# Kernel tuning notes

Measured on AMD Instinct MI355X. Metric: run time of the kernel, lower is better.

## Reference

```python
import jax, jax.numpy as jnp
import numpy as np

I, H, O = 32, 64, 8  # input_size, hidden_layer, output_size
B, T = 4096, 256


def setup_inputs() -> dict:
    key = jax.random.key(0)
    ks = jax.random.split(key, 7)
    s_ih = 1.0 / np.sqrt(H)
    return {
        "x": jax.random.normal(ks[0], (B, T, I), dtype=jnp.float32),
        # PyTorch nn.LSTM params, gate order [i, f, g, o]
        "W_ih": jax.random.uniform(ks[1], (4 * H, I), jnp.float32, -s_ih, s_ih),
        "W_hh": jax.random.uniform(ks[2], (4 * H, H), jnp.float32, -s_ih, s_ih),
        "b_ih": jax.random.uniform(ks[3], (4 * H,), jnp.float32, -s_ih, s_ih),
        "b_hh": jax.random.uniform(ks[4], (4 * H,), jnp.float32, -s_ih, s_ih),
        "W_fc": jax.random.uniform(ks[5], (O, H), jnp.float32, -s_ih, s_ih),
        "b_fc": jax.random.uniform(ks[6], (O,), jnp.float32, -s_ih, s_ih),
    }


def reference(x, W_ih, W_hh, b_ih, b_hh, W_fc, b_fc):
    # Precompute input-to-hidden projections for all timesteps in one GEMM.
    # [B, T, 4H]
    x_proj = jnp.einsum('bti,gi->btg', x, W_ih) + b_ih + b_hh

    def step(carry, xp_t):
        h, c = carry  # [B, H] each
        gates = xp_t + h @ W_hh.T  # [B, 4H]
        i_g, f_g, g_g, o_g = jnp.split(gates, 4, axis=-1)
        i_g = jax.nn.sigmoid(i_g)
        f_g = jax.nn.sigmoid(f_g)
        g_g = jnp.tanh(g_g)
        o_g = jax.nn.sigmoid(o_g)
        c = f_g * c + i_g * g_g
        h = o_g * jnp.tanh(c)
        return (h, c), None

    h0 = jnp.zeros((x.shape[0], H), dtype=x.dtype)
    c0 = jnp.zeros((x.shape[0], H), dtype=x.dtype)
    # scan over time axis: move T to leading axis
    (h_T, c_T), _ = jax.lax.scan(step, (h0, c0), jnp.swapaxes(x_proj, 0, 1))
    # out[:, -1, :] == final hidden state for single-layer batch_first LSTM
    return h_T @ W_fc.T + b_fc
```

## Files before the change

### kernel.cpp

```cpp
#include <hip/hip_runtime.h>
#include <hip/hip_bf16.h>


#define T_LEN 256
#define I_SZ  32
#define H_SZ  64
#define O_SZ  8
#define BR    8
#define HS    72

typedef __attribute__((ext_vector_type(8))) short short8;
typedef __attribute__((ext_vector_type(4))) float f32x4;
typedef __attribute__((ext_vector_type(2))) float f32x2;

static __device__ __forceinline__ unsigned fbits(float f) {
    union { float f; unsigned u; } v; v.f = f; return v.u;
}
static __device__ __forceinline__ unsigned pk2t(float lo, float hi) {
    return __builtin_amdgcn_perm(fbits(hi), fbits(lo), 0x07060302u);
}
static __device__ __forceinline__ short f2bf_rne(float f) {
    union { __hip_bfloat16 b; short s; } u;
    u.b = __float2bfloat16(f);
    return u.s;
}
static __device__ __forceinline__ f32x2 rcp2(f32x2 d) {
    f32x2 r;
    r.x = __builtin_amdgcn_rcpf(d.x);
    r.y = __builtin_amdgcn_rcpf(d.y);
    return r;
}
static __device__ __forceinline__ f32x2 fma2(f32x2 a, f32x2 b, f32x2 c) {
    return __builtin_elementwise_fma(a, b, c);
}
static __device__ __forceinline__ f32x2 tanh2(f32x2 x) {
    f32x2 x2 = x * x;
    f32x2 n  = fma2(x2 + 105.0f, x2, (f32x2)(945.0f));
    f32x2 d  = fma2(fma2((f32x2)(15.0f), x2, (f32x2)(420.0f)), x2, (f32x2)(945.0f));
    f32x2 r  = (x * n) * rcp2(d);
    r = __builtin_elementwise_min(r, (f32x2)(1.0f));
    r = __builtin_elementwise_max(r, (f32x2)(-1.0f));
    return r;
}
static __device__ __forceinline__ f32x2 sig2(f32x2 x) {
    f32x2 x2 = x * x;
    f32x2 n  = fma2(x2 + 420.0f, x2, (f32x2)(15120.0f));
    f32x2 d  = fma2(fma2((f32x2)(60.0f), x2, (f32x2)(6720.0f)), x2, (f32x2)(60480.0f));
    f32x2 r  = fma2(x * n, rcp2(d), (f32x2)(0.5f));
    r = __builtin_elementwise_min(r, (f32x2)(1.0f));
    r = __builtin_elementwise_max(r, (f32x2)(0.0f));
    return r;
}

__global__ __launch_bounds__(256, 2)
void lstm_fused_kernel(const float* __restrict__ x,
                       const float* __restrict__ W_ih,
                       const float* __restrict__ W_hh,
                       const float* __restrict__ b_ih,
                       const float* __restrict__ b_hh,
                       const float* __restrict__ W_fc,
                       const float* __restrict__ b_fc,
                       float* __restrict__ out)
{
    __shared__ short hbuf[2][8][HS];
    __shared__ float Hf[BR][64];

    const int tid  = threadIdx.x;
    const int wave = tid >> 6;
    const int lane = tid & 63;
    const int quad = lane >> 4;
    const int nlow = lane & 15;
    const int jw   = wave * 16 + nlow;
    const int b0   = blockIdx.x * BR;

    const int fr = (nlow < 8) ? nlow : (((nlow & 4) ? 6 : 2) + (nlow & 1));
    const int ra = ((quad & 1) << 2) | (quad & 2);

    short8 bfrag[4][3];
    f32x4  biasf[4];
    for (int g = 0; g < 4; ++g) {
        const int col = g * 64 + jw;
        {
            const float* wr = W_ih + col * I_SZ + quad * 8;
            short8 f;
            #pragma unroll
            for (int e = 0; e < 8; ++e) f[e] = f2bf_rne(wr[e]);
            bfrag[g][0] = f;
        }
        #pragma unroll
        for (int kt = 1; kt < 3; ++kt) {
            const float* wr = W_hh + col * H_SZ + (kt - 1) * 32 + quad * 8;
            short8 f;
            #pragma unroll
            for (int e = 0; e < 8; ++e) f[e] = f2bf_rne(wr[e]);
            bfrag[g][kt] = f;
        }
        const float bg = b_ih[col] + b_hh[col];
        biasf[g] = (f32x4){bg, bg, bg, bg};
    }

    for (int q = tid; q < 2 * 8 * HS; q += 256) ((short*)hbuf)[q] = (short)0;

    const float* xb = x + ((size_t)(b0 + fr) * T_LEN) * I_SZ + quad * 8;

    float4 nx[16];
    short8 sc[8];
    #pragma unroll
    for (int s = 0; s < 8; ++s) {
        nx[2*s]   = *(const float4*)(xb + s * I_SZ);
        nx[2*s+1] = *(const float4*)(xb + s * I_SZ + 4);
    }
    #pragma unroll
    for (int s = 0; s < 8; ++s) {
        union { uint4 u; short8 v; } w;
        w.u.x = pk2t(nx[2*s].x,   nx[2*s].y);
        w.u.y = pk2t(nx[2*s].z,   nx[2*s].w);
        w.u.z = pk2t(nx[2*s+1].x, nx[2*s+1].y);
        w.u.w = pk2t(nx[2*s+1].z, nx[2*s+1].w);
        sc[s] = w.v;
    }

    const short* rb[2] = { &hbuf[0][fr][quad * 8], &hbuf[1][fr][quad * 8] };
    short*       wb[2] = { &hbuf[0][ra][jw],       &hbuf[1][ra][jw] };

    f32x2 cc = {0.f, 0.f};
    f32x2 hh = {0.f, 0.f};

    for (int ch = 0; ch < 32; ++ch) {
        #pragma unroll
        for (int tc = 0; tc < 8; ++tc) {
            const int t = ch * 8 + tc;

            __syncthreads();

            const short* hr = rb[t & 1];
            short8 a1 = *(const short8*)(hr);
            short8 a2 = *(const short8*)(hr + 32);

            if (tc == 0 && ch + 1 < 32) {
                const float* nxt = xb + (t + 8) * I_SZ;
                #pragma unroll
                for (int s = 0; s < 8; ++s) {
                    nx[2*s]   = *(const float4*)(nxt + s * I_SZ);
                    nx[2*s+1] = *(const float4*)(nxt + s * I_SZ + 4);
                }
            }

            const short8 ax = sc[tc];

            f32x4 acc[4];
            #pragma unroll
            for (int g = 0; g < 4; ++g) {
                f32x4 a = __builtin_amdgcn_mfma_f32_16x16x32_bf16(ax, bfrag[g][0], biasf[g], 0, 0, 0);
                a = __builtin_amdgcn_mfma_f32_16x16x32_bf16(a1, bfrag[g][1], a, 0, 0, 0);
                a = __builtin_amdgcn_mfma_f32_16x16x32_bf16(a2, bfrag[g][2], a, 0, 0, 0);
                acc[g] = a;
            }

            if (tc == 7 && ch + 1 < 32) {
                #pragma unroll
                for (int s = 0; s < 8; ++s) {
                    union { uint4 u; short8 v; } w;
                    w.u.x = pk2t(nx[2*s].x,   nx[2*s].y);
                    w.u.y = pk2t(nx[2*s].z,   nx[2*s].w);
                    w.u.z = pk2t(nx[2*s+1].x, nx[2*s+1].y);
                    w.u.w = pk2t(nx[2*s+1].z, nx[2*s+1].w);
                    sc[s] = w.v;
                }
            }

            f32x2 pI = {acc[0][0], acc[0][1]};
            f32x2 pF = {acc[1][0], acc[1][1]};
            f32x2 pG = {acc[2][0], acc[2][1]};
            f32x2 pO = {acc[3][0], acc[3][1]};

            f32x2 iv = sig2(pI);
            f32x2 fv = sig2(pF);
            f32x2 gv = tanh2(pG);
            f32x2 ov = sig2(pO);
            cc = fma2(fv, cc, iv * gv);
            hh = ov * tanh2(cc);

            short* hw = wb[(t + 1) & 1];
            hw[0]  = (short)((fbits(hh.x) + 0x8000u) >> 16);
            hw[HS] = (short)((fbits(hh.y) + 0x8000u) >> 16);
        }
    }

    Hf[ra][jw]     = hh.x;
    Hf[ra + 1][jw] = hh.y;
    __syncthreads();

    if (tid < BR * O_SZ) {
        const int r = tid >> 3;
        const int o = tid & 7;
        const float* wf = W_fc + o * H_SZ;
        float acc = b_fc[o];
        #pragma unroll
        for (int jx = 0; jx < H_SZ; ++jx) acc += Hf[r][jx] * wf[jx];
        out[(size_t)(b0 + r) * O_SZ + o] = acc;
    }
}

extern "C" void kernel_launch(void* const* d_in, const int* in_sizes, int n_in,
                              void* d_out, int out_size, void* d_ws, size_t ws_size,
                              hipStream_t stream) {
    const float* x    = (const float*)d_in[0];
    const float* W_ih = (const float*)d_in[1];
    const float* W_hh = (const float*)d_in[2];
    const float* b_ih = (const float*)d_in[3];
    const float* b_hh = (const float*)d_in[4];
    const float* W_fc = (const float*)d_in[5];
    const float* b_fc = (const float*)d_in[6];
    float* out = (float*)d_out;

    const int B = 4096;
    lstm_fused_kernel<<<dim3(B / BR), dim3(256), 0, stream>>>(
        x, W_ih, W_hh, b_ih, b_hh, W_fc, b_fc, out);
}
```

Baseline: 318.4 us.

## Halve batch rows per block and double resident blocks per CU

```diff
diff --git a/kernel.cpp b/kernel.cpp
--- a/kernel.cpp
+++ b/kernel.cpp
@@ -6,12 +6,11 @@
 #define I_SZ  32
 #define H_SZ  64
 #define O_SZ  8
-#define BR    8
+#define BR    4
 #define HS    72
 
 typedef __attribute__((ext_vector_type(8))) short short8;
 typedef __attribute__((ext_vector_type(4))) float f32x4;
-typedef __attribute__((ext_vector_type(2))) float f32x2;
 
 static __device__ __forceinline__ unsigned fbits(float f) {
     union { float f; unsigned u; } v; v.f = f; return v.u;
@@ -24,35 +23,22 @@
     u.b = __float2bfloat16(f);
     return u.s;
 }
-static __device__ __forceinline__ f32x2 rcp2(f32x2 d) {
-    f32x2 r;
-    r.x = __builtin_amdgcn_rcpf(d.x);
-    r.y = __builtin_amdgcn_rcpf(d.y);
-    return r;
+static __device__ __forceinline__ float tanh_p(float x) {
+    float x2 = x * x;
+    float n  = fmaf(x2 + 105.0f, x2, 945.0f);
+    float d  = fmaf(fmaf(15.0f, x2, 420.0f), x2, 945.0f);
+    float r  = (x * n) * __builtin_amdgcn_rcpf(d);
+    return fminf(fmaxf(r, -1.0f), 1.0f);
 }
-static __device__ __forceinline__ f32x2 fma2(f32x2 a, f32x2 b, f32x2 c) {
-    return __builtin_elementwise_fma(a, b, c);
-}
-static __device__ __forceinline__ f32x2 tanh2(f32x2 x) {
-    f32x2 x2 = x * x;
-    f32x2 n  = fma2(x2 + 105.0f, x2, (f32x2)(945.0f));
-    f32x2 d  = fma2(fma2((f32x2)(15.0f), x2, (f32x2)(420.0f)), x2, (f32x2)(945.0f));
-    f32x2 r  = (x * n) * rcp2(d);
-    r = __builtin_elementwise_min(r, (f32x2)(1.0f));
-    r = __builtin_elementwise_max(r, (f32x2)(-1.0f));
-    return r;
-}
-static __device__ __forceinline__ f32x2 sig2(f32x2 x) {
-    f32x2 x2 = x * x;
-    f32x2 n  = fma2(x2 + 420.0f, x2, (f32x2)(15120.0f));
-    f32x2 d  = fma2(fma2((f32x2)(60.0f), x2, (f32x2)(6720.0f)), x2, (f32x2)(60480.0f));
-    f32x2 r  = fma2(x * n, rcp2(d), (f32x2)(0.5f));
-    r = __builtin_elementwise_min(r, (f32x2)(1.0f));
-    r = __builtin_elementwise_max(r, (f32x2)(0.0f));
-    return r;
+static __device__ __forceinline__ float sig_p(float x) {
+    float x2 = x * x;
+    float n  = fmaf(x2 + 420.0f, x2, 15120.0f);
+    float d  = fmaf(fmaf(60.0f, x2, 6720.0f), x2, 60480.0f);
+    float r  = fmaf(x * n, __builtin_amdgcn_rcpf(d), 0.5f);
+    return fminf(fmaxf(r, 0.0f), 1.0f);
 }
 
-__global__ __launch_bounds__(256, 2)
+__global__ __launch_bounds__(256, 4)
 void lstm_fused_kernel(const float* __restrict__ x,
                        const float* __restrict__ W_ih,
                        const float* __restrict__ W_hh,
@@ -62,7 +48,7 @@
                        const float* __restrict__ b_fc,
                        float* __restrict__ out)
 {
-    __shared__ short hbuf[2][8][HS];
+    __shared__ short hbuf[2][BR][HS];
     __shared__ float Hf[BR][64];
 
     const int tid  = threadIdx.x;
@@ -73,8 +59,7 @@
     const int jw   = wave * 16 + nlow;
     const int b0   = blockIdx.x * BR;
 
-    const int fr = (nlow < 8) ? nlow : (((nlow & 4) ? 6 : 2) + (nlow & 1));
-    const int ra = ((quad & 1) << 2) | (quad & 2);
+    const int fr = nlow >> 2;
 
     short8 bfrag[4][3];
     f32x4  biasf[4];
@@ -99,19 +84,19 @@
         biasf[g] = (f32x4){bg, bg, bg, bg};
     }
 
-    for (int q = tid; q < 2 * 8 * HS; q += 256) ((short*)hbuf)[q] = (short)0;
+    for (int q = tid; q < 2 * BR * HS; q += 256) ((short*)hbuf)[q] = (short)0;
 
     const float* xb = x + ((size_t)(b0 + fr) * T_LEN) * I_SZ + quad * 8;
 
-    float4 nx[16];
-    short8 sc[8];
+    float4 nx[8];
+    short8 sc[4];
     #pragma unroll
-    for (int s = 0; s < 8; ++s) {
+    for (int s = 0; s < 4; ++s) {
         nx[2*s]   = *(const float4*)(xb + s * I_SZ);
         nx[2*s+1] = *(const float4*)(xb + s * I_SZ + 4);
     }
     #pragma unroll
-    for (int s = 0; s < 8; ++s) {
+    for (int s = 0; s < 4; ++s) {
         union { uint4 u; short8 v; } w;
         w.u.x = pk2t(nx[2*s].x,   nx[2*s].y);
         w.u.y = pk2t(nx[2*s].z,   nx[2*s].w);
@@ -121,15 +106,14 @@
     }
 
     const short* rb[2] = { &hbuf[0][fr][quad * 8], &hbuf[1][fr][quad * 8] };
-    short*       wb[2] = { &hbuf[0][ra][jw],       &hbuf[1][ra][jw] };
+    short*       wb[2] = { &hbuf[0][quad][jw],     &hbuf[1][quad][jw] };
 
-    f32x2 cc = {0.f, 0.f};
-    f32x2 hh = {0.f, 0.f};
+    float cc = 0.f, hh = 0.f;
 
-    for (int ch = 0; ch < 32; ++ch) {
+    for (int ch = 0; ch < 64; ++ch) {
         #pragma unroll
-        for (int tc = 0; tc < 8; ++tc) {
-            const int t = ch * 8 + tc;
+        for (int tc = 0; tc < 4; ++tc) {
+            const int t = ch * 4 + tc;
 
             __syncthreads();
 
@@ -137,10 +121,10 @@
             short8 a1 = *(const short8*)(hr);
             short8 a2 = *(const short8*)(hr + 32);
 
-            if (tc == 0 && ch + 1 < 32) {
-                const float* nxt = xb + (t + 8) * I_SZ;
+            if (tc == 0 && ch + 1 < 64) {
+                const float* nxt = xb + (t + 4) * I_SZ;
                 #pragma unroll
-                for (int s = 0; s < 8; ++s) {
+                for (int s = 0; s < 4; ++s) {
                     nx[2*s]   = *(const float4*)(nxt + s * I_SZ);
                     nx[2*s+1] = *(const float4*)(nxt + s * I_SZ + 4);
                 }
@@ -157,9 +141,9 @@
                 acc[g] = a;
             }
 
-            if (tc == 7 && ch + 1 < 32) {
+            if (tc == 3 && ch + 1 < 64) {
                 #pragma unroll
-                for (int s = 0; s < 8; ++s) {
+                for (int s = 0; s < 4; ++s) {
                     union { uint4 u; short8 v; } w;
                     w.u.x = pk2t(nx[2*s].x,   nx[2*s].y);
                     w.u.y = pk2t(nx[2*s].z,   nx[2*s].w);
@@ -169,26 +153,18 @@
                 }
             }
 
-            f32x2 pI = {acc[0][0], acc[0][1]};
-            f32x2 pF = {acc[1][0], acc[1][1]};
-            f32x2 pG = {acc[2][0], acc[2][1]};
-            f32x2 pO = {acc[3][0], acc[3][1]};
+            float iv = sig_p(acc[0][0]);
+            float fv = sig_p(acc[1][0]);
+            float gv = tanh_p(acc[2][0]);
+            float ov = sig_p(acc[3][0]);
+            cc = fmaf(fv, cc, iv * gv);
+            hh = ov * tanh_p(cc);
 
-            f32x2 iv = sig2(pI);
-            f32x2 fv = sig2(pF);
-            f32x2 gv = tanh2(pG);
-            f32x2 ov = sig2(pO);
-            cc = fma2(fv, cc, iv * gv);
-            hh = ov * tanh2(cc);
-
-            short* hw = wb[(t + 1) & 1];
-            hw[0]  = (short)((fbits(hh.x) + 0x8000u) >> 16);
-            hw[HS] = (short)((fbits(hh.y) + 0x8000u) >> 16);
+            wb[(t + 1) & 1][0] = (short)((fbits(hh) + 0x8000u) >> 16);
         }
     }
 
-    Hf[ra][jw]     = hh.x;
-    Hf[ra + 1][jw] = hh.y;
+    Hf[quad][jw] = hh;
     __syncthreads();
 
     if (tid < BR * O_SZ) {
```

Result: slower. 606.4 us (+90.5%).
